# Performance work log

Measured on AMD Instinct MI355X. Metric: run time of the kernel, lower is better.

## Reference

```python
import jax, jax.numpy as jnp
import numpy as np

C_LOGIT = 10.0  # logit range hyperparameter (use_tanh=True)


def setup_inputs() -> dict:
    key = jax.random.key(0)
    ks = jax.random.split(key, 7)
    B, S, D = 64, 2048, 512
    s = 1.0 / np.sqrt(D)
    return {
        "query": jax.random.normal(ks[0], (B, D), jnp.float32),
        "ref": jax.random.normal(ks[1], (B, S, D), jnp.float32),
        "Wq_w": jax.random.uniform(ks[2], (D, D), jnp.float32, -s, s),
        "Wq_b": jax.random.uniform(ks[3], (D,), jnp.float32, -s, s),
        "Wr_w": jax.random.uniform(ks[4], (D, D), jnp.float32, -s, s),  # Conv1d k=1 == Linear
        "Wr_b": jax.random.uniform(ks[5], (D,), jnp.float32, -s, s),
        "value": jax.random.uniform(ks[6], (D,), jnp.float32, -s, s),
    }


def reference(query, ref, Wq_w, Wq_b, Wr_w, Wr_b, value):
    # query: [B, D], ref: [B, S, D]
    q = query @ Wq_w.T + Wq_b                                  # [B, D]  (Wq linear)
    r = jnp.einsum("bsd,ed->bse", ref, Wr_w) + Wr_b            # [B, S, D] (Conv1d k=1 over permuted ref)
    h = jnp.tanh(q[:, None, :] + r)                            # broadcast query over seq_len
    logits = jnp.einsum("bsd,d->bs", h, value)                 # <v, tanh(Wq q + Wr r)>
    logits = C_LOGIT * jnp.tanh(logits)                        # use_tanh=True
    ref_out = jnp.transpose(r, (0, 2, 1))                      # [B, D, S] as returned by torch branch
    return ref_out, logits
```

## Files before the change

### kernel.cpp

```cpp
#include <hip/hip_runtime.h>
#include <stdint.h>

#define NB  64
#define SEQ 2048
#define DIM 512
#define NS  (NB*SEQ)

typedef __bf16 bf16x8 __attribute__((ext_vector_type(8)));
typedef float  f32x4  __attribute__((ext_vector_type(4)));
typedef unsigned int u32;
typedef unsigned short u16;
typedef unsigned int u32x2 __attribute__((ext_vector_type(2)));
typedef unsigned int u32x4 __attribute__((ext_vector_type(4)));

__device__ __forceinline__ u32 pk_bf16(float a, float b){
  union {float f; u32 i;} x, y; x.f = a; y.f = b;
  return ((x.i + 0x8000u) >> 16) | ((y.i + 0x8000u) & 0xffff0000u);
}
__device__ __forceinline__ float fast_tanh(float x){
  float e = __builtin_amdgcn_exp2f(x * 2.885390081777927f);
  return 1.0f - 2.0f*__builtin_amdgcn_rcpf(e + 1.0f);
}
__device__ __forceinline__ void gload_lds16(const void* g, void* l){
  __builtin_amdgcn_global_load_lds((const __attribute__((address_space(1))) void*)g,
                                   (__attribute__((address_space(3))) void*)l, 16, 0, 0);
}

__global__ void wconv_kernel(const float* __restrict__ Wr_w, u16* __restrict__ wrbf)
{
  const int i = blockIdx.x*256 + threadIdx.x;
  f32x4 v = ((const f32x4*)Wr_w)[i];
  u32x2 p; p.x = pk_bf16(v.x, v.y); p.y = pk_bf16(v.z, v.w);
  ((u32x2*)wrbf)[i] = p;
}

__global__ void q_kernel(const float* __restrict__ query, const float* __restrict__ Wq_w,
                         const float* __restrict__ Wq_b, float* __restrict__ qws)
{
  __shared__ float lq[DIM];
  const int b   = blockIdx.x;
  const int tid = threadIdx.x;
  const int e   = blockIdx.y*256 + tid;
  for (int i = tid; i < DIM; i += 256) lq[i] = query[b*DIM + i];
  __syncthreads();
  const float* wr = Wq_w + (size_t)e*DIM;
  float acc = 0.f;
  for (int d = 0; d < DIM; d += 4){
    f32x4 w = *(const f32x4*)(wr + d);
    acc += w.x*lq[d] + w.y*lq[d+1] + w.z*lq[d+2] + w.w*lq[d+3];
  }
  qws[b*DIM + e] = acc + Wq_b[e];
}

#define BN 64
#define ET 128
#define BK 32

__global__ __launch_bounds__(256)
void main_kernel(const float* __restrict__ ref,  const u16* __restrict__ wrbf,
                 const float* __restrict__ Wr_b, const float* __restrict__ value,
                 const float* __restrict__ qws,  float* __restrict__ out)
{
  __shared__ __align__(16) char smem[81920];
  char* refL = smem;
  char* wb0  = smem + 65536;
  char* wb1  = smem + 65536 + 8192;

  const int tid  = threadIdx.x;
  const int lane = tid & 63, wave = tid >> 6;
  const int col  = lane & 15, quad = lane >> 4;
  const size_t s0 = (size_t)blockIdx.x * BN;
  const int b  = (int)(s0 >> 11);
  const int sb = (int)(s0 & 2047);

  auto stage_w = [&](char* dst, int c){
    const int et = c >> 4, kt = c & 15;
#pragma unroll
    for (int j = 0; j < 2; ++j){
      const int idx = j*256 + wave*64 + lane;
      const int er  = et*ET + (idx >> 2);
      const u16* g  = wrbf + (size_t)er*DIM + kt*BK + (idx & 3)*8;
      gload_lds16(g, dst + (size_t)idx*16);
    }
  };

  stage_w(wb0, 0);

  for (int it = 0; it < 16; ++it){
    const int c   = it*256 + tid;
    const int row = c >> 6, ch = c & 63;
    const float* g = ref + (s0 + row)*DIM + ch*8;
    f32x4 x0 = *(const f32x4*)g, x1 = *(const f32x4*)(g+4);
    u32x4 p;
    p[0]=pk_bf16(x0.x,x0.y); p[1]=pk_bf16(x0.z,x0.w);
    p[2]=pk_bf16(x1.x,x1.y); p[3]=pk_bf16(x1.z,x1.w);
    *(u32x4*)(refL + row*1024 + ((ch ^ (row&7)))*16) = p;
  }
  __syncthreads();

  f32x4 acc[2][4];
#pragma unroll
  for (int mi = 0; mi < 2; ++mi)
#pragma unroll
    for (int ni = 0; ni < 4; ++ni) acc[mi][ni] = (f32x4)0.0f;
  float lsum[4] = {0.f, 0.f, 0.f, 0.f};

  char* wcur = wb0;
  char* wnxt = wb1;

  for (int c = 0; c < 64; ++c){
    if (c + 1 < 64) stage_w(wnxt, c + 1);

    const int kt = c & 15;
    bf16x8 af[2], bfr[4];
#pragma unroll
    for (int mi = 0; mi < 2; ++mi)
      af[mi] = *(const bf16x8*)(wcur + (wave*32 + mi*16 + col)*64 + quad*16);
#pragma unroll
    for (int ni = 0; ni < 4; ++ni){
      const int r = ni*16 + col;
      bfr[ni] = *(const bf16x8*)(refL + r*1024 + (((kt*4 + quad) ^ (r&7)))*16);
    }
#pragma unroll
    for (int mi = 0; mi < 2; ++mi)
#pragma unroll
      for (int ni = 0; ni < 4; ++ni)
        acc[mi][ni] = __builtin_amdgcn_mfma_f32_16x16x32_bf16(af[mi], bfr[ni], acc[mi][ni], 0, 0, 0);

    if (kt == 15){
      const int et = c >> 4;
#pragma unroll
      for (int mi = 0; mi < 2; ++mi){
#pragma unroll
        for (int rg = 0; rg < 4; ++rg){
          const int eg = et*ET + wave*32 + mi*16 + quad*4 + rg;
          const float bias = Wr_b[eg];
          const float qe   = qws[b*DIM + eg];
          const float val  = value[eg];
          float* orow = out + ((size_t)(b*DIM + eg))*SEQ + sb;
#pragma unroll
          for (int ni = 0; ni < 4; ++ni){
            const float r = acc[mi][ni][rg] + bias;
            orow[ni*16 + col] = r;
            lsum[ni] += fast_tanh(qe + r) * val;
          }
        }
      }
#pragma unroll
      for (int mi = 0; mi < 2; ++mi)
#pragma unroll
        for (int ni = 0; ni < 4; ++ni) acc[mi][ni] = (f32x4)0.0f;
    }

    __syncthreads();
    char* t = wcur; wcur = wnxt; wnxt = t;
  }

#pragma unroll
  for (int ni = 0; ni < 4; ++ni){
    lsum[ni] += __shfl_xor(lsum[ni], 16);
    lsum[ni] += __shfl_xor(lsum[ni], 32);
  }
  float* lred = (float*)(smem + 65536);
  if (quad == 0){
#pragma unroll
    for (int ni = 0; ni < 4; ++ni) lred[wave*64 + ni*16 + col] = lsum[ni];
  }
  __syncthreads();
  if (tid < BN){
    const float s = lred[tid] + lred[64+tid] + lred[128+tid] + lred[192+tid];
    out[(size_t)NB*DIM*SEQ + b*SEQ + sb + tid] = 10.0f * fast_tanh(s);
  }
}

extern "C" void kernel_launch(void* const* d_in, const int* in_sizes, int n_in,
                              void* d_out, int out_size, void* d_ws, size_t ws_size,
                              hipStream_t stream)
{
  const float* query = (const float*)d_in[0];
  const float* ref   = (const float*)d_in[1];
  const float* Wq_w  = (const float*)d_in[2];
  const float* Wq_b  = (const float*)d_in[3];
  const float* Wr_w  = (const float*)d_in[4];
  const float* Wr_b  = (const float*)d_in[5];
  const float* value = (const float*)d_in[6];
  float* out = (float*)d_out;

  float* qws  = (float*)d_ws;
  u16*   wrbf = (u16*)((float*)d_ws + NB*DIM);

  wconv_kernel<<<dim3(256), dim3(256), 0, stream>>>(Wr_w, wrbf);
  q_kernel<<<dim3(NB, 2), dim3(256), 0, stream>>>(query, Wq_w, Wq_b, qws);
  main_kernel<<<dim3(NS/BN), dim3(256), 0, stream>>>(ref, wrbf, Wr_b, value, qws, out);
}
```

Measured before the change: 541.4 us.

## Pre-swizzle bf16 weights into MFMA fragment order and load them directly to registers

```diff
diff --git a/kernel.cpp b/kernel.cpp
--- a/kernel.cpp
+++ b/kernel.cpp
@@ -10,7 +10,6 @@
 typedef float  f32x4  __attribute__((ext_vector_type(4)));
 typedef unsigned int u32;
 typedef unsigned short u16;
-typedef unsigned int u32x2 __attribute__((ext_vector_type(2)));
 typedef unsigned int u32x4 __attribute__((ext_vector_type(4)));
 
 __device__ __forceinline__ u32 pk_bf16(float a, float b){
@@ -21,17 +20,17 @@
   float e = __builtin_amdgcn_exp2f(x * 2.885390081777927f);
   return 1.0f - 2.0f*__builtin_amdgcn_rcpf(e + 1.0f);
 }
-__device__ __forceinline__ void gload_lds16(const void* g, void* l){
-  __builtin_amdgcn_global_load_lds((const __attribute__((address_space(1))) void*)g,
-                                   (__attribute__((address_space(3))) void*)l, 16, 0, 0);
-}
 
 __global__ void wconv_kernel(const float* __restrict__ Wr_w, u16* __restrict__ wrbf)
 {
   const int i = blockIdx.x*256 + threadIdx.x;
-  f32x4 v = ((const f32x4*)Wr_w)[i];
-  u32x2 p; p.x = pk_bf16(v.x, v.y); p.y = pk_bf16(v.z, v.w);
-  ((u32x2*)wrbf)[i] = p;
+  const int eb = i >> 10, kt = (i >> 6) & 15, quad = (i >> 4) & 3, col = i & 15;
+  const float* g = Wr_w + (size_t)(eb*16 + col)*DIM + kt*32 + quad*8;
+  f32x4 a = *(const f32x4*)g, c = *(const f32x4*)(g + 4);
+  u32x4 p;
+  p[0]=pk_bf16(a.x,a.y); p[1]=pk_bf16(a.z,a.w);
+  p[2]=pk_bf16(c.x,c.y); p[3]=pk_bf16(c.z,c.w);
+  ((u32x4*)wrbf)[i] = p;
 }
 
 __global__ void q_kernel(const float* __restrict__ query, const float* __restrict__ Wq_w,
@@ -53,18 +52,15 @@
 }
 
 #define BN 64
-#define ET 128
-#define BK 32
 
-__global__ __launch_bounds__(256)
+__global__ __launch_bounds__(256, 2)
 void main_kernel(const float* __restrict__ ref,  const u16* __restrict__ wrbf,
                  const float* __restrict__ Wr_b, const float* __restrict__ value,
                  const float* __restrict__ qws,  float* __restrict__ out)
 {
-  __shared__ __align__(16) char smem[81920];
-  char* refL = smem;
-  char* wb0  = smem + 65536;
-  char* wb1  = smem + 65536 + 8192;
+  __shared__ __align__(16) char smem[66560];
+  char*  refL = smem;
+  float* lred = (float*)(smem + 65536);
 
   const int tid  = threadIdx.x;
   const int lane = tid & 63, wave = tid >> 6;
@@ -73,19 +69,7 @@
   const int b  = (int)(s0 >> 11);
   const int sb = (int)(s0 & 2047);
 
-  auto stage_w = [&](char* dst, int c){
-    const int et = c >> 4, kt = c & 15;
-#pragma unroll
-    for (int j = 0; j < 2; ++j){
-      const int idx = j*256 + wave*64 + lane;
-      const int er  = et*ET + (idx >> 2);
-      const u16* g  = wrbf + (size_t)er*DIM + kt*BK + (idx & 3)*8;
-      gload_lds16(g, dst + (size_t)idx*16);
-    }
-  };
-
-  stage_w(wb0, 0);
-
+#pragma unroll 4
   for (int it = 0; it < 16; ++it){
     const int c   = it*256 + tid;
     const int row = c >> 6, ch = c & 63;
@@ -94,77 +78,94 @@
     u32x4 p;
     p[0]=pk_bf16(x0.x,x0.y); p[1]=pk_bf16(x0.z,x0.w);
     p[2]=pk_bf16(x1.x,x1.y); p[3]=pk_bf16(x1.z,x1.w);
-    *(u32x4*)(refL + row*1024 + ((ch ^ (row&7)))*16) = p;
+    *(u32x4*)(refL + row*1024 + (ch ^ (row&7))*16) = p;
   }
   __syncthreads();
 
-  f32x4 acc[2][4];
+  f32x4 acc[4][2][4];
 #pragma unroll
-  for (int mi = 0; mi < 2; ++mi)
-#pragma unroll
-    for (int ni = 0; ni < 4; ++ni) acc[mi][ni] = (f32x4)0.0f;
-  float lsum[4] = {0.f, 0.f, 0.f, 0.f};
-
-  char* wcur = wb0;
-  char* wnxt = wb1;
-
-  for (int c = 0; c < 64; ++c){
-    if (c + 1 < 64) stage_w(wnxt, c + 1);
-
-    const int kt = c & 15;
-    bf16x8 af[2], bfr[4];
+  for (int et = 0; et < 4; ++et)
 #pragma unroll
     for (int mi = 0; mi < 2; ++mi)
-      af[mi] = *(const bf16x8*)(wcur + (wave*32 + mi*16 + col)*64 + quad*16);
+#pragma unroll
+      for (int ni = 0; ni < 4; ++ni) acc[et][mi][ni] = (f32x4)0.0f;
+
+  auto wptr = [&](int et, int mi, int kt){
+    const int eb = et*8 + wave*2 + mi;
+    return (const bf16x8*)(wrbf + ((size_t)((eb*16 + kt)*64 + lane))*8);
+  };
+
+  bf16x8 wbuf[2][2];
+  wbuf[0][0] = *wptr(0, 0, 0);
+  wbuf[0][1] = *wptr(0, 1, 0);
+  bf16x8 rf[4];
+
+  for (int kt = 0; kt < 16; ++kt){
 #pragma unroll
     for (int ni = 0; ni < 4; ++ni){
       const int r = ni*16 + col;
-      bfr[ni] = *(const bf16x8*)(refL + r*1024 + (((kt*4 + quad) ^ (r&7)))*16);
+      rf[ni] = *(const bf16x8*)(refL + r*1024 + (((kt*4 + quad) ^ (r&7)))*16);
     }
 #pragma unroll
-    for (int mi = 0; mi < 2; ++mi)
-#pragma unroll
-      for (int ni = 0; ni < 4; ++ni)
-        acc[mi][ni] = __builtin_amdgcn_mfma_f32_16x16x32_bf16(af[mi], bfr[ni], acc[mi][ni], 0, 0, 0);
-
-    if (kt == 15){
-      const int et = c >> 4;
-#pragma unroll
-      for (int mi = 0; mi < 2; ++mi){
-#pragma unroll
-        for (int rg = 0; rg < 4; ++rg){
-          const int eg = et*ET + wave*32 + mi*16 + quad*4 + rg;
-          const float bias = Wr_b[eg];
-          const float qe   = qws[b*DIM + eg];
-          const float val  = value[eg];
-          float* orow = out + ((size_t)(b*DIM + eg))*SEQ + sb;
-#pragma unroll
-          for (int ni = 0; ni < 4; ++ni){
-            const float r = acc[mi][ni][rg] + bias;
-            orow[ni*16 + col] = r;
-            lsum[ni] += fast_tanh(qe + r) * val;
-          }
-        }
+    for (int et = 0; et < 4; ++et){
+      const int p = et & 1;
+      if (!(kt == 15 && et == 3)){
+        const int ne = (et + 1) & 3, nk = (et == 3) ? kt + 1 : kt;
+        wbuf[p^1][0] = *wptr(ne, 0, nk);
+        wbuf[p^1][1] = *wptr(ne, 1, nk);
       }
 #pragma unroll
       for (int mi = 0; mi < 2; ++mi)
 #pragma unroll
-        for (int ni = 0; ni < 4; ++ni) acc[mi][ni] = (f32x4)0.0f;
+        for (int ni = 0; ni < 4; ++ni)
+          acc[et][mi][ni] = __builtin_amdgcn_mfma_f32_16x16x32_bf16(
+                              rf[ni], wbuf[p][mi], acc[et][mi][ni], 0, 0, 0);
     }
+  }
 
-    __syncthreads();
-    char* t = wcur; wcur = wnxt; wnxt = t;
+  float ls[4][4];
+#pragma unroll
+  for (int ni = 0; ni < 4; ++ni)
+#pragma unroll
+    for (int rg = 0; rg < 4; ++rg) ls[ni][rg] = 0.f;
+
+#pragma unroll
+  for (int et = 0; et < 4; ++et){
+#pragma unroll
+    for (int mi = 0; mi < 2; ++mi){
+      const int e = et*128 + wave*32 + mi*16 + col;
+      const float bb = Wr_b[e];
+      const float qq = qws[b*DIM + e];
+      const float vv = value[e];
+      float* orow = out + ((size_t)(b*DIM + e))*SEQ + sb + quad*4;
+#pragma unroll
+      for (int ni = 0; ni < 4; ++ni){
+        f32x4 v = acc[et][mi][ni];
+        v.x += bb; v.y += bb; v.z += bb; v.w += bb;
+        *(f32x4*)(orow + ni*16) = v;
+        ls[ni][0] += fast_tanh(qq + v.x) * vv;
+        ls[ni][1] += fast_tanh(qq + v.y) * vv;
+        ls[ni][2] += fast_tanh(qq + v.z) * vv;
+        ls[ni][3] += fast_tanh(qq + v.w) * vv;
+      }
+    }
   }
 
 #pragma unroll
-  for (int ni = 0; ni < 4; ++ni){
-    lsum[ni] += __shfl_xor(lsum[ni], 16);
-    lsum[ni] += __shfl_xor(lsum[ni], 32);
-  }
-  float* lred = (float*)(smem + 65536);
-  if (quad == 0){
+  for (int ni = 0; ni < 4; ++ni)
 #pragma unroll
-    for (int ni = 0; ni < 4; ++ni) lred[wave*64 + ni*16 + col] = lsum[ni];
+    for (int rg = 0; rg < 4; ++rg){
+      float x = ls[ni][rg];
+      x += __shfl_xor(x, 1); x += __shfl_xor(x, 2);
+      x += __shfl_xor(x, 4); x += __shfl_xor(x, 8);
+      ls[ni][rg] = x;
+    }
+  if (col == 0){
+#pragma unroll
+    for (int ni = 0; ni < 4; ++ni)
+#pragma unroll
+      for (int rg = 0; rg < 4; ++rg)
+        lred[wave*64 + ni*16 + quad*4 + rg] = ls[ni][rg];
   }
   __syncthreads();
   if (tid < BN){
@@ -189,7 +190,7 @@
   float* qws  = (float*)d_ws;
   u16*   wrbf = (u16*)((float*)d_ws + NB*DIM);
 
-  wconv_kernel<<<dim3(256), dim3(256), 0, stream>>>(Wr_w, wrbf);
+  wconv_kernel<<<dim3(128), dim3(256), 0, stream>>>(Wr_w, wrbf);
   q_kernel<<<dim3(NB, 2), dim3(256), 0, stream>>>(query, Wq_w, Wq_b, qws);
   main_kernel<<<dim3(NS/BN), dim3(256), 0, stream>>>(ref, wrbf, Wr_b, value, qws, out);
 }
```

After: 534.8 us. Within noise of the previous version (-1.2%).
